# Kernel optimization log

Hardware: AMD Instinct MI355X
Metric: run time of the kernel (lower is better)

The kernel has to match this reference:

```python
import jax, jax.numpy as jnp
import numpy as np

H = 8   # n_heads
C = 2   # top-k scale factor: topk = int(C * log(L))


def setup_inputs() -> dict:
    key = jax.random.key(0)
    k1, k2, k3 = jax.random.split(key, 3)
    B, L, D = 16, 512, 4096  # L == D // H required by the original broadcasting
    Q = jax.random.normal(k1, (B, L, D), dtype=jnp.float32)
    K = jax.random.normal(k2, (B, L, D), dtype=jnp.float32)
    V = jax.random.normal(k3, (B, L, D), dtype=jnp.float32)
    return {"Q": Q, "K": K, "V": V}


def _autocorrelation(Q, K, V):
    B, L, D = Q.shape
    d = D // H
    # [B,L,D] -> [B,H,L,d]
    q = Q.reshape(B, L, H, d).transpose(0, 2, 1, 3)
    k = K.reshape(B, L, H, d).transpose(0, 2, 1, 3)
    v = V.reshape(B, L, H, d).transpose(0, 2, 1, 3)
    # FFT-based autocorrelation along the time axis (per head, per channel)
    qf = jnp.fft.fft(q, axis=2)
    kf = jnp.fft.fft(k, axis=2)
    corr = jnp.fft.ifft(qf * jnp.conj(kf), axis=2).real  # [B,H,L,d]
    topk = int(C * np.log(L))  # static: 12 for L=512
    # top-k delays per (batch, head, channel): move L to last axis
    w, idx = jax.lax.top_k(corr.transpose(0, 1, 3, 2), topk)  # [B,H,d,topk]
    w = jax.nn.softmax(w, axis=-1)
    pos = jnp.arange(L)[:, None]  # [L,1]
    out = jnp.zeros_like(v)       # [B,H,L,d]
    # small fixed loop over topk ~ O(log L) delays: gather + scale + accumulate
    for i in range(topk):
        g = jnp.minimum(idx[:, :, None, :, i] + pos, L - 1)        # [B,H,L,d]
        out = out + w[:, :, None, :, i] * jnp.take_along_axis(v, g, axis=2)
    return out.transpose(0, 2, 1, 3).reshape(B, L, D)


def reference(Q, K, V):
    return _autocorrelation(Q, K, V)
```

## Files before the change

kernel.cpp:

```cpp
#include <hip/hip_runtime.h>

#define L_LEN 512
#define D_DIM 4096
#define H_NUM 8
#define B_NUM 16
#define TOPK  12


#define QLD(GI) (qc4[(GI) ^ (((GI) >> 3) & 1)])

#define ITER(P, I) do {                                                      \
    const int gb = 4 * (I) + 8;                                              \
    const float4 r0_ = QLD(gq + gb);                                         \
    const float4 r1_ = QLD(gq + gb + 1);                                     \
    const float4 r2_ = QLD(gq + gb + 2);                                     \
    const float4 r3_ = QLD(gq + gb + 3);                                     \
    const float4 ka_ = kc4[4 * (I)];                                         \
    const float4 kb_ = kc4[4 * (I) + 1];                                     \
    {                                                                        \
      const float kk[8] = {ka_.x,ka_.y,ka_.z,ka_.w, kb_.x,kb_.y,kb_.z,kb_.w};\
      _Pragma("unroll")                                                      \
      for (int tt = 0; tt < 8; ++tt)                                         \
        _Pragma("unroll")                                                    \
        for (int ii = 0; ii < 8; ++ii)                                       \
          acc[ii] = fmaf(qb[((P) + ii + tt) & 31], kk[tt], acc[ii]);         \
    }                                                                        \
    const float4 kc_ = kc4[4 * (I) + 2];                                     \
    const float4 kd_ = kc4[4 * (I) + 3];                                     \
    {                                                                        \
      const float kk[8] = {kc_.x,kc_.y,kc_.z,kc_.w, kd_.x,kd_.y,kd_.z,kd_.w};\
      _Pragma("unroll")                                                      \
      for (int tt = 0; tt < 8; ++tt)                                         \
        _Pragma("unroll")                                                    \
        for (int ii = 0; ii < 8; ++ii)                                       \
          acc[ii] = fmaf(qb[((P) + 8 + ii + tt) & 31], kk[tt], acc[ii]);     \
    }                                                                        \
    qb[(P)+ 0]=r0_.x; qb[(P)+ 1]=r0_.y; qb[(P)+ 2]=r0_.z; qb[(P)+ 3]=r0_.w;  \
    qb[(P)+ 4]=r1_.x; qb[(P)+ 5]=r1_.y; qb[(P)+ 6]=r1_.z; qb[(P)+ 7]=r1_.w;  \
    qb[(P)+ 8]=r2_.x; qb[(P)+ 9]=r2_.y; qb[(P)+10]=r2_.z; qb[(P)+11]=r2_.w;  \
    qb[(P)+12]=r3_.x; qb[(P)+13]=r3_.y; qb[(P)+14]=r3_.z; qb[(P)+15]=r3_.w;  \
  } while (0)

__global__ __launch_bounds__(512, 4) void corr_topk_kernel(
    const float* __restrict__ Q, const float* __restrict__ K,
    float* __restrict__ ws_w, int* __restrict__ ws_i)
{
  __shared__ __align__(16) float qs[8][1056];
  __shared__ __align__(16) float ks[8][512];

  const int tid = threadIdx.x;
  const int bid = blockIdx.x;
  const int work = (bid & 7) * 1024 + (bid >> 3);
  const int bh   = work >> 6;
  const int c0   = (work & 63) * 8;

  const size_t base = (size_t)(bh >> 3) * (size_t)(L_LEN * D_DIM)
                    + (size_t)(bh & 7) * 512 + c0;

  #pragma unroll
  for (int rep = 0; rep < 2; ++rep) {
    const int idx  = rep * 512 + tid;
    const int t    = idx >> 1;
    const int half = idx & 1;
    const float4 qv = *(const float4*)(Q + base + (size_t)t * D_DIM + half * 4);
    const float4 kv = *(const float4*)(K + base + (size_t)t * D_DIM + half * 4);
    const int pw = ((((t >> 2) ^ ((t >> 5) & 1)) << 2) | (t & 3));
    const int cb = half * 4;
    const float qa[4] = {qv.x, qv.y, qv.z, qv.w};
    const float ka[4] = {kv.x, kv.y, kv.z, kv.w};
    #pragma unroll
    for (int j = 0; j < 4; ++j) {
      qs[cb + j][pw]       = qa[j];
      qs[cb + j][pw + 512] = qa[j];
      ks[cb + j][t]        = ka[j];
    }
    if (t < 32) {
      #pragma unroll
      for (int j = 0; j < 4; ++j) qs[cb + j][pw + 1024] = qa[j];
    }
  }
  __syncthreads();

  const int wv   = __builtin_amdgcn_readfirstlane(tid >> 6);
  const int lane = tid & 63;
  const int tau0 = lane * 8;
  const int gq   = lane * 2;

  const float4* __restrict__ qc4 = (const float4*)qs[wv];
  const float4* __restrict__ kc4 = (const float4*)ks[wv];

  float acc[8];
  #pragma unroll
  for (int i = 0; i < 8; ++i) acc[i] = 0.f;

  float qb[32];
  #pragma unroll
  for (int x = 0; x < 8; ++x) {
    const float4 v = QLD(gq + x);
    qb[4*x] = v.x; qb[4*x+1] = v.y; qb[4*x+2] = v.z; qb[4*x+3] = v.w;
  }

  #pragma unroll 1
  for (int i = 0; i < 32; i += 2) {
    ITER(0, i);
    ITER(16, i + 1);
  }

  float bv[TOPK]; int bi[TOPK];
  #pragma unroll
  for (int s = 0; s < TOPK; ++s) {
    float lv = acc[0]; int li = 0;
    #pragma unroll
    for (int i = 1; i < 8; ++i) if (acc[i] > lv) { lv = acc[i]; li = i; }
    int gi = tau0 + li;
    #pragma unroll
    for (int off = 32; off >= 1; off >>= 1) {
      const float ov = __shfl_xor(lv, off, 64);
      const int   oi = __shfl_xor(gi, off, 64);
      if (ov > lv || (ov == lv && oi < gi)) { lv = ov; gi = oi; }
    }
    bv[s] = lv; bi[s] = gi;
    const int slot = gi - tau0;
    #pragma unroll
    for (int i = 0; i < 8; ++i) acc[i] = (slot == i) ? -3.4e38f : acc[i];
  }

  float e[TOPK]; float sum = 0.f;
  #pragma unroll
  for (int s = 0; s < TOPK; ++s) { e[s] = expf(bv[s] - bv[0]); sum += e[s]; }
  const float inv = 1.f / sum;

  if (lane == 0) {
    const int g = (bh * 512 + c0 + wv) * TOPK;
    #pragma unroll
    for (int s = 0; s < TOPK; ++s) { ws_w[g + s] = e[s] * inv; ws_i[g + s] = bi[s]; }
  }
}

__global__ __launch_bounds__(512, 4) void gather_kernel(
    const float* __restrict__ V, const float* __restrict__ ws_w,
    const int* __restrict__ ws_i, float* __restrict__ out)
{
  __shared__ __align__(16) float vs[512][32];

  const int tid = threadIdx.x;
  const int bid = blockIdx.x;
  const int work = (bid & 7) * 256 + (bid >> 3);
  const int b  = work >> 7;
  const int dg = work & 127;
  const int d0 = dg * 32;
  const int h  = d0 >> 9;
  const int c0 = d0 & 511;

  const size_t vcol = (size_t)b * (size_t)(L_LEN * D_DIM) + d0;

  const int cl   = tid & 31;
  const int tsub = tid >> 5;

  float4 stga, stgb;
  const int e0 = tid, e1 = 512 + tid;
  const int ra0 = e0 >> 3, qa0 = (e0 & 7) * 4;
  const int rb0 = e1 >> 3, qb0 = (e1 & 7) * 4;

  stga = *(const float4*)(V + vcol + (size_t)(384 + ra0) * D_DIM + qa0);
  stgb = *(const float4*)(V + vcol + (size_t)(384 + rb0) * D_DIM + qb0);

  const int g = ((b * 8 + h) * 512 + c0 + cl) * TOPK;
  float w[TOPK]; int r0[TOPK];
  #pragma unroll
  for (int s = 0; s < TOPK; ++s) { w[s] = ws_w[g + s]; r0[s] = ws_i[g + s]; }

  const size_t ob = vcol + cl;

  #pragma unroll 1
  for (int ph = 3; ph >= 0; --ph) {
    *(float4*)(&vs[ph * 128 + ra0][qa0]) = stga;
    *(float4*)(&vs[ph * 128 + rb0][qb0]) = stgb;
    if (ph > 0) {
      stga = *(const float4*)(V + vcol + (size_t)((ph - 1) * 128 + ra0) * D_DIM + qa0);
      stgb = *(const float4*)(V + vcol + (size_t)((ph - 1) * 128 + rb0) * D_DIM + qb0);
    }
    asm volatile("s_waitcnt lgkmcnt(0)" ::: "memory");
    __builtin_amdgcn_s_barrier();
    asm volatile("" ::: "memory");

    #pragma unroll
    for (int k8 = 0; k8 < 8; ++k8) {
      const int t = ph * 128 + (k8 << 4) + tsub;
      float a = 0.f;
      #pragma unroll
      for (int s = 0; s < TOPK; ++s) {
        int r = r0[s] + t;
        r = r > (L_LEN - 1) ? (L_LEN - 1) : r;
        a = fmaf(w[s], vs[r][cl], a);
      }
      out[ob + (size_t)t * D_DIM] = a;
    }
  }
}

extern "C" void kernel_launch(void* const* d_in, const int* in_sizes, int n_in,
                              void* d_out, int out_size, void* d_ws, size_t ws_size,
                              hipStream_t stream)
{
  const float* Q = (const float*)d_in[0];
  const float* K = (const float*)d_in[1];
  const float* V = (const float*)d_in[2];
  float* out = (float*)d_out;

  float* ws_w = (float*)d_ws;
  int*   ws_i = (int*)((char*)d_ws + (size_t)B_NUM * H_NUM * 512 * TOPK * sizeof(float));

  corr_topk_kernel<<<dim3(B_NUM * H_NUM * 64), dim3(512), 0, stream>>>(Q, K, ws_w, ws_i);
  gather_kernel<<<dim3(B_NUM * H_NUM * 16), dim3(512), 0, stream>>>(V, ws_w, ws_i, out);
}
```

Baseline: 854.1 us.

## Rewrite correlation inner loop with inline-asm LDS reads and rotating register windows

Replaces the doubled/tripled Q shared-memory copy with a single padded copy that uses modular wraparound addressing. It also switches the inner correlation loop to hand-written ds_read_b128 inline assembly with a three-way rotating register window and named accumulators. The goal is to cut LDS footprint and per-block staging writes, allowing more occupancy, and to shrink the register shuffling the compiler generated for the circular q buffer. The risk is that each iteration ends with a full lgkmcnt(0) wait, which serializes LDS latency against the FMAs and may stall more than before.

```diff
diff --git a/kernel.cpp b/kernel.cpp
--- a/kernel.cpp
+++ b/kernel.cpp
@@ -1,4 +1,5 @@
 #include <hip/hip_runtime.h>
+#include <stdint.h>
 
 #define L_LEN 512
 #define D_DIM 4096
@@ -6,46 +7,61 @@
 #define B_NUM 16
 #define TOPK  12
 
-
-#define QLD(GI) (qc4[(GI) ^ (((GI) >> 3) & 1)])
-
-#define ITER(P, I) do {                                                      \
-    const int gb = 4 * (I) + 8;                                              \
-    const float4 r0_ = QLD(gq + gb);                                         \
-    const float4 r1_ = QLD(gq + gb + 1);                                     \
-    const float4 r2_ = QLD(gq + gb + 2);                                     \
-    const float4 r3_ = QLD(gq + gb + 3);                                     \
-    const float4 ka_ = kc4[4 * (I)];                                         \
-    const float4 kb_ = kc4[4 * (I) + 1];                                     \
-    {                                                                        \
-      const float kk[8] = {ka_.x,ka_.y,ka_.z,ka_.w, kb_.x,kb_.y,kb_.z,kb_.w};\
-      _Pragma("unroll")                                                      \
-      for (int tt = 0; tt < 8; ++tt)                                         \
-        _Pragma("unroll")                                                    \
-        for (int ii = 0; ii < 8; ++ii)                                       \
-          acc[ii] = fmaf(qb[((P) + ii + tt) & 31], kk[tt], acc[ii]);         \
-    }                                                                        \
-    const float4 kc_ = kc4[4 * (I) + 2];                                     \
-    const float4 kd_ = kc4[4 * (I) + 3];                                     \
-    {                                                                        \
-      const float kk[8] = {kc_.x,kc_.y,kc_.z,kc_.w, kd_.x,kd_.y,kd_.z,kd_.w};\
-      _Pragma("unroll")                                                      \
-      for (int tt = 0; tt < 8; ++tt)                                         \
-        _Pragma("unroll")                                                    \
-        for (int ii = 0; ii < 8; ++ii)                                       \
-          acc[ii] = fmaf(qb[((P) + 8 + ii + tt) & 31], kk[tt], acc[ii]);     \
-    }                                                                        \
-    qb[(P)+ 0]=r0_.x; qb[(P)+ 1]=r0_.y; qb[(P)+ 2]=r0_.z; qb[(P)+ 3]=r0_.w;  \
-    qb[(P)+ 4]=r1_.x; qb[(P)+ 5]=r1_.y; qb[(P)+ 6]=r1_.z; qb[(P)+ 7]=r1_.w;  \
-    qb[(P)+ 8]=r2_.x; qb[(P)+ 9]=r2_.y; qb[(P)+10]=r2_.z; qb[(P)+11]=r2_.w;  \
-    qb[(P)+12]=r3_.x; qb[(P)+13]=r3_.y; qb[(P)+14]=r3_.z; qb[(P)+15]=r3_.w;  \
+typedef float f32x4 __attribute__((ext_vector_type(4)));
+
+
+#define QA(G) (qbase + (((((uint32_t)(G)) & 127u) + ((((uint32_t)(G)) & 127u) >> 3)) << 4))
+
+#define MAC4x8(QA_, QB_, QC_, KK_) do {                                       \
+    acc0 = fmaf(QA_.x, KK_.x, acc0); acc0 = fmaf(QA_.y, KK_.y, acc0);         \
+    acc0 = fmaf(QA_.z, KK_.z, acc0); acc0 = fmaf(QA_.w, KK_.w, acc0);         \
+    acc1 = fmaf(QA_.y, KK_.x, acc1); acc1 = fmaf(QA_.z, KK_.y, acc1);         \
+    acc1 = fmaf(QA_.w, KK_.z, acc1); acc1 = fmaf(QB_.x, KK_.w, acc1);         \
+    acc2 = fmaf(QA_.z, KK_.x, acc2); acc2 = fmaf(QA_.w, KK_.y, acc2);         \
+    acc2 = fmaf(QB_.x, KK_.z, acc2); acc2 = fmaf(QB_.y, KK_.w, acc2);         \
+    acc3 = fmaf(QA_.w, KK_.x, acc3); acc3 = fmaf(QB_.x, KK_.y, acc3);         \
+    acc3 = fmaf(QB_.y, KK_.z, acc3); acc3 = fmaf(QB_.z, KK_.w, acc3);         \
+    acc4 = fmaf(QB_.x, KK_.x, acc4); acc4 = fmaf(QB_.y, KK_.y, acc4);         \
+    acc4 = fmaf(QB_.z, KK_.z, acc4); acc4 = fmaf(QB_.w, KK_.w, acc4);         \
+    acc5 = fmaf(QB_.y, KK_.x, acc5); acc5 = fmaf(QB_.z, KK_.y, acc5);         \
+    acc5 = fmaf(QB_.w, KK_.z, acc5); acc5 = fmaf(QC_.x, KK_.w, acc5);         \
+    acc6 = fmaf(QB_.z, KK_.x, acc6); acc6 = fmaf(QB_.w, KK_.y, acc6);         \
+    acc6 = fmaf(QC_.x, KK_.z, acc6); acc6 = fmaf(QC_.y, KK_.w, acc6);         \
+    acc7 = fmaf(QB_.w, KK_.x, acc7); acc7 = fmaf(QC_.x, KK_.y, acc7);         \
+    acc7 = fmaf(QC_.y, KK_.z, acc7); acc7 = fmaf(QC_.z, KK_.w, acc7);         \
+  } while (0)
+
+#define ITER3(A0,A1,A2,A3, B0,B1,B2,B3, C0,C1,C2,C3) do {                    \
+    const uint32_t a0_ = QA(gnext);                                          \
+    const uint32_t a1_ = QA(gnext + 1);                                      \
+    const uint32_t a2_ = QA(gnext + 2);                                      \
+    const uint32_t a3_ = QA(gnext + 3);                                      \
+    asm volatile(                                                            \
+      "ds_read_b128 %0, %8\n\t"                                              \
+      "ds_read_b128 %1, %9\n\t"                                              \
+      "ds_read_b128 %2, %10\n\t"                                             \
+      "ds_read_b128 %3, %11\n\t"                                             \
+      "ds_read_b128 %4, %12\n\t"                                             \
+      "ds_read_b128 %5, %12 offset:16\n\t"                                   \
+      "ds_read_b128 %6, %12 offset:32\n\t"                                   \
+      "ds_read_b128 %7, %12 offset:48\n\t"                                   \
+      "s_waitcnt lgkmcnt(0)"                                                 \
+      : "=&v"(C0), "=&v"(C1), "=&v"(C2), "=&v"(C3),                          \
+        "=&v"(k0), "=&v"(k1), "=&v"(k2), "=&v"(k3)                           \
+      : "v"(a0_), "v"(a1_), "v"(a2_), "v"(a3_), "v"(kcur)                    \
+      : "memory");                                                           \
+    MAC4x8(A0, A1, A2, k0);                                                  \
+    MAC4x8(A1, A2, A3, k1);                                                  \
+    MAC4x8(A2, A3, B0, k2);                                                  \
+    MAC4x8(A3, B0, B1, k3);                                                  \
+    gnext += 4; kcur += 64;                                                  \
   } while (0)
 
 __global__ __launch_bounds__(512, 4) void corr_topk_kernel(
     const float* __restrict__ Q, const float* __restrict__ K,
     float* __restrict__ ws_w, int* __restrict__ ws_i)
 {
-  __shared__ __align__(16) float qs[8][1056];
+  __shared__ __align__(16) float qs[8][576];
   __shared__ __align__(16) float ks[8][512];
 
   const int tid = threadIdx.x;
@@ -64,19 +80,15 @@
     const int half = idx & 1;
     const float4 qv = *(const float4*)(Q + base + (size_t)t * D_DIM + half * 4);
     const float4 kv = *(const float4*)(K + base + (size_t)t * D_DIM + half * 4);
-    const int pw = ((((t >> 2) ^ ((t >> 5) & 1)) << 2) | (t & 3));
+    const int g  = t >> 2;
+    const int pw = ((g + (g >> 3)) << 2) | (t & 3);
     const int cb = half * 4;
     const float qa[4] = {qv.x, qv.y, qv.z, qv.w};
     const float ka[4] = {kv.x, kv.y, kv.z, kv.w};
     #pragma unroll
     for (int j = 0; j < 4; ++j) {
-      qs[cb + j][pw]       = qa[j];
-      qs[cb + j][pw + 512] = qa[j];
-      ks[cb + j][t]        = ka[j];
-    }
-    if (t < 32) {
-      #pragma unroll
-      for (int j = 0; j < 4; ++j) qs[cb + j][pw + 1024] = qa[j];
+      qs[cb + j][pw] = qa[j];
+      ks[cb + j][t]  = ka[j];
     }
   }
   __syncthreads();
@@ -86,25 +98,48 @@
   const int tau0 = lane * 8;
   const int gq   = lane * 2;
 
-  const float4* __restrict__ qc4 = (const float4*)qs[wv];
-  const float4* __restrict__ kc4 = (const float4*)ks[wv];
-
-  float acc[8];
-  #pragma unroll
-  for (int i = 0; i < 8; ++i) acc[i] = 0.f;
-
-  float qb[32];
-  #pragma unroll
-  for (int x = 0; x < 8; ++x) {
-    const float4 v = QLD(gq + x);
-    qb[4*x] = v.x; qb[4*x+1] = v.y; qb[4*x+2] = v.z; qb[4*x+3] = v.w;
-  }
+  const uint32_t qbase = (uint32_t)(uintptr_t)(&qs[wv][0]);
+  const uint32_t kbase = (uint32_t)(uintptr_t)(&ks[wv][0]);
+
+  float acc0 = 0.f, acc1 = 0.f, acc2 = 0.f, acc3 = 0.f;
+  float acc4 = 0.f, acc5 = 0.f, acc6 = 0.f, acc7 = 0.f;
+  f32x4 wA0, wA1, wA2, wA3, wB0, wB1, wB2, wB3, wC0, wC1, wC2, wC3;
+  f32x4 k0, k1, k2, k3;
+
+  {
+    const uint32_t p0 = QA(gq),     p1 = QA(gq + 1);
+    const uint32_t p2 = QA(gq + 2), p3 = QA(gq + 3);
+    const uint32_t p4 = QA(gq + 4), p5 = QA(gq + 5);
+    const uint32_t p6 = QA(gq + 6), p7 = QA(gq + 7);
+    asm volatile(
+      "ds_read_b128 %0, %8\n\t"
+      "ds_read_b128 %1, %9\n\t"
+      "ds_read_b128 %2, %10\n\t"
+      "ds_read_b128 %3, %11\n\t"
+      "ds_read_b128 %4, %12\n\t"
+      "ds_read_b128 %5, %13\n\t"
+      "ds_read_b128 %6, %14\n\t"
+      "ds_read_b128 %7, %15\n\t"
+      "s_waitcnt lgkmcnt(0)"
+      : "=&v"(wA0), "=&v"(wA1), "=&v"(wA2), "=&v"(wA3),
+        "=&v"(wB0), "=&v"(wB1), "=&v"(wB2), "=&v"(wB3)
+      : "v"(p0), "v"(p1), "v"(p2), "v"(p3), "v"(p4), "v"(p5), "v"(p6), "v"(p7)
+      : "memory");
+  }
+
+  uint32_t gnext = (uint32_t)(gq + 8);
+  uint32_t kcur  = kbase;
 
   #pragma unroll 1
-  for (int i = 0; i < 32; i += 2) {
-    ITER(0, i);
-    ITER(16, i + 1);
-  }
+  for (int i = 0; i < 30; i += 3) {
+    ITER3(wA0,wA1,wA2,wA3, wB0,wB1,wB2,wB3, wC0,wC1,wC2,wC3);
+    ITER3(wB0,wB1,wB2,wB3, wC0,wC1,wC2,wC3, wA0,wA1,wA2,wA3);
+    ITER3(wC0,wC1,wC2,wC3, wA0,wA1,wA2,wA3, wB0,wB1,wB2,wB3);
+  }
+  ITER3(wA0,wA1,wA2,wA3, wB0,wB1,wB2,wB3, wC0,wC1,wC2,wC3);
+  ITER3(wB0,wB1,wB2,wB3, wC0,wC1,wC2,wC3, wA0,wA1,wA2,wA3);
+
+  float acc[8] = {acc0, acc1, acc2, acc3, acc4, acc5, acc6, acc7};
 
   float bv[TOPK]; int bi[TOPK];
   #pragma unroll
```

New measurement: 836.8 us. 1.02x faster.
